# Optimization experiments

Measured on AMD Instinct MI355X. Metric: run time of the kernel, lower is better.

## Reference

```python
import jax, jax.numpy as jnp
import numpy as np
from jax import lax

B, DIM, H, W = 16, 256, 56, 56
HEADS, WIN, K = 8, 4, 5
DH = DIM // HEADS
BN_EPS = 1e-5


def conv2d(x, w, b, stride=1, pad=0, groups=1):
    y = lax.conv_general_dilated(
        x, w, (stride, stride), [(pad, pad), (pad, pad)],
        dimension_numbers=('NCHW', 'OIHW', 'NCHW'), feature_group_count=groups)
    return y + b[None, :, None, None]


def batchnorm(x, g, b, m, v):
    scale = g / jnp.sqrt(v + BN_EPS)
    return (x - m[None, :, None, None]) * scale[None, :, None, None] + b[None, :, None, None]


def setup_inputs() -> dict:
    key = jax.random.key(0)
    ks = jax.random.split(key, 16)
    s = 0.05
    return {
        'x': jax.random.normal(ks[0], (B, DIM, H, W), jnp.float32),
        'q_w': jax.random.normal(ks[1], (DIM, DIM, 1, 1), jnp.float32) * s,
        'q_b': jnp.zeros((DIM,), jnp.float32),
        'kv_w': jax.random.normal(ks[2], (2 * DIM, DIM, 1, 1), jnp.float32) * s,
        'kv_b': jnp.zeros((2 * DIM,), jnp.float32),
        'p0_w': jax.random.normal(ks[3], (DIM, 1, K, K), jnp.float32) * s,
        'p0_b': jnp.zeros((DIM,), jnp.float32),
        'bn0_g': jnp.ones((DIM,), jnp.float32),
        'bn0_b': jnp.zeros((DIM,), jnp.float32),
        'bn0_m': jax.random.normal(ks[4], (DIM,), jnp.float32) * 0.1,
        'bn0_v': jax.random.uniform(ks[5], (DIM,), jnp.float32, 0.5, 1.5),
        'pl0_w': jax.random.normal(ks[6], (DIM, DIM, 1, 1), jnp.float32) * s,
        'pl0_b': jnp.zeros((DIM,), jnp.float32),
        'p1_w': jax.random.normal(ks[7], (DIM, 1, K, K), jnp.float32) * s,
        'p1_b': jnp.zeros((DIM,), jnp.float32),
        'bn1_g': jnp.ones((DIM,), jnp.float32),
        'bn1_b': jnp.zeros((DIM,), jnp.float32),
        'bn1_m': jax.random.normal(ks[8], (DIM,), jnp.float32) * 0.1,
        'bn1_v': jax.random.uniform(ks[9], (DIM,), jnp.float32, 0.5, 1.5),
        'loc_w': jax.random.normal(ks[10], (DIM, 1, K, K), jnp.float32) * s,
        'loc_b': jnp.zeros((DIM,), jnp.float32),
        'mix_w': jax.random.normal(ks[11], (DIM, DIM, 1, 1), jnp.float32) * s,
        'mix_b': jnp.zeros((DIM,), jnp.float32),
    }


def reference(x, q_w, q_b, kv_w, kv_b, p0_w, p0_b, bn0_g, bn0_b, bn0_m, bn0_v,
              pl0_w, pl0_b, p1_w, p1_b, bn1_g, bn1_b, bn1_m, bn1_v,
              loc_w, loc_b, mix_w, mix_b):
    b, c, h, w = x.shape
    scalor = DH ** (-0.5)

    # Q projection (1x1 conv)
    q_local = conv2d(x, q_w, q_b)

    # refined_downsample: (dwconv s2 -> BN -> 1x1) -> (dwconv s2 -> BN)
    p = conv2d(x, p0_w, p0_b, stride=2, pad=K // 2, groups=DIM)
    p = batchnorm(p, bn0_g, bn0_b, bn0_m, bn0_v)
    p = conv2d(p, pl0_w, pl0_b)
    p = conv2d(p, p1_w, p1_b, stride=2, pad=K // 2, groups=DIM)
    p = batchnorm(p, bn1_g, bn1_b, bn1_m, bn1_v)
    Hp, Wp = p.shape[2], p.shape[3]

    # KV projection on pooled map
    kv = conv2d(p, kv_w, kv_b)  # (b, 2*c, Hp, Wp)
    kv = kv.reshape(b, 2, HEADS, DH, Hp * Wp)
    k = kv[:, 0].transpose(0, 1, 3, 2)  # (b, heads, HW, dh)
    v = kv[:, 1].transpose(0, 1, 3, 2)

    q = q_local.reshape(b, HEADS, DH, h * w).transpose(0, 1, 3, 2)  # (b, heads, hw, dh)

    attn = jax.nn.softmax(scalor * jnp.einsum('bnqd,bnkd->bnqk', q, k), axis=-1)
    global_feat = jnp.einsum('bnqk,bnkd->bnqd', attn, v)  # (b, heads, hw, dh)
    global_feat = global_feat.transpose(0, 1, 3, 2).reshape(b, c, h, w)

    # local mixer: depthwise conv (use_lfae=False path)
    local_feat = conv2d(q_local, loc_w, loc_b, pad=K // 2, groups=DIM)
    local_feat = local_feat * jax.nn.sigmoid(local_feat)  # local_weight gating (silu)
    local_feat = local_feat * jax.nn.sigmoid(global_feat)  # local2global gating

    return conv2d(local_feat * global_feat, mix_w, mix_b)
```

## Files before the change

kernel.cpp:

```cpp
#include <hip/hip_runtime.h>
#include <cstdint>

#define BEPS 1e-5f

typedef __attribute__((ext_vector_type(8))) short short8;
typedef __attribute__((ext_vector_type(4))) float f32x4;

static __device__ __forceinline__ uint32_t f2bf(float f) {
    union { float f; uint32_t u; } v; v.f = f;
    return (v.u + 0x7FFFu + ((v.u >> 16) & 1u)) >> 16;
}
static __device__ __forceinline__ uint32_t pk2(float lo, float hi) {
    return (f2bf(hi) << 16) | (f2bf(lo) & 0xFFFFu);
}

__global__ __launch_bounds__(256) void gemm1x1_mfma(
    const float* __restrict__ in, const float* __restrict__ w,
    const float* __restrict__ bias, float* __restrict__ out,
    int Ci, int Co, int P)
{
    const int b  = blockIdx.z;
    const int p0 = blockIdx.x * 128;
    const int c0 = blockIdx.y * 128;
    const int tid  = threadIdx.x;
    const int lane = tid & 63;
    const int wave = tid >> 6;
    const int wm = wave >> 1, wn = wave & 1;
    const int l15 = lane & 15;
    const int kg  = lane >> 4;

    __shared__ short sA[128][40];
    __shared__ short sB[128][40];

    f32x4 acc[4][4] = {};

    const float* inb = in + (size_t)b * Ci * P;

    const int arow  = tid >> 1;
    const int ahalf = (tid & 1) * 16;
    const int bp    = tid & 127;
    const int bhalf = (tid >> 7) * 16;
    const bool bok  = (p0 + bp) < P;

    for (int k0 = 0; k0 < Ci; k0 += 32) {
        {
            const float* src = &w[(size_t)(c0 + arow) * Ci + k0 + ahalf];
            float4 f0 = *(const float4*)(src + 0);
            float4 f1 = *(const float4*)(src + 4);
            float4 f2 = *(const float4*)(src + 8);
            float4 f3 = *(const float4*)(src + 12);
            uint4 q0, q1;
            q0.x = pk2(f0.x, f0.y); q0.y = pk2(f0.z, f0.w);
            q0.z = pk2(f1.x, f1.y); q0.w = pk2(f1.z, f1.w);
            q1.x = pk2(f2.x, f2.y); q1.y = pk2(f2.z, f2.w);
            q1.z = pk2(f3.x, f3.y); q1.w = pk2(f3.z, f3.w);
            *(uint4*)&sA[arow][ahalf]     = q0;
            *(uint4*)&sA[arow][ahalf + 8] = q1;
        }
        {
            const float* src = &inb[(size_t)(k0 + bhalf) * P + p0 + bp];
            float fv[16];
#pragma unroll
            for (int i = 0; i < 16; ++i)
                fv[i] = bok ? src[(size_t)i * P] : 0.f;
            uint4 q0, q1;
            q0.x = pk2(fv[0], fv[1]);  q0.y = pk2(fv[2], fv[3]);
            q0.z = pk2(fv[4], fv[5]);  q0.w = pk2(fv[6], fv[7]);
            q1.x = pk2(fv[8], fv[9]);  q1.y = pk2(fv[10], fv[11]);
            q1.z = pk2(fv[12], fv[13]); q1.w = pk2(fv[14], fv[15]);
            *(uint4*)&sB[bp][bhalf]     = q0;
            *(uint4*)&sB[bp][bhalf + 8] = q1;
        }
        __syncthreads();

        short8 aF[4], bF[4];
#pragma unroll
        for (int m = 0; m < 4; ++m)
            aF[m] = *(const short8*)&sA[wm * 64 + m * 16 + l15][kg * 8];
#pragma unroll
        for (int n = 0; n < 4; ++n)
            bF[n] = *(const short8*)&sB[wn * 64 + n * 16 + l15][kg * 8];
#pragma unroll
        for (int m = 0; m < 4; ++m)
#pragma unroll
            for (int n = 0; n < 4; ++n)
                acc[m][n] = __builtin_amdgcn_mfma_f32_16x16x32_bf16(aF[m], bF[n], acc[m][n], 0, 0, 0);
        __syncthreads();
    }

    float* outb = out + (size_t)b * Co * P;
#pragma unroll
    for (int m = 0; m < 4; ++m) {
        int row = c0 + wm * 64 + m * 16 + kg * 4;
#pragma unroll
        for (int n = 0; n < 4; ++n) {
            int col = p0 + wn * 64 + n * 16 + l15;
            if (col < P) {
#pragma unroll
                for (int j = 0; j < 4; ++j)
                    outb[(size_t)(row + j) * P + col] = acc[m][n][j] + bias[row + j];
            }
        }
    }
}

__global__ __launch_bounds__(256) void dwconv_bn(
    const float* __restrict__ in, const float* __restrict__ w5,
    const float* __restrict__ cb, const float* __restrict__ g,
    const float* __restrict__ bb, const float* __restrict__ m,
    const float* __restrict__ v, float* __restrict__ out,
    int Hin, int Win, int Hout, int Wout, int stride, int total)
{
    int idx = blockIdx.x * 256 + threadIdx.x;
    if (idx >= total) return;
    int x = idx % Wout;
    int t = idx / Wout;
    int y = t % Hout;
    t /= Hout;
    int c = t & 255;
    int b = t >> 8;
    const float* ib = in + (size_t)(b * 256 + c) * Hin * Win;
    const float* wc = w5 + c * 25;
    float s = 0.f;
#pragma unroll
    for (int dy = 0; dy < 5; ++dy) {
        int iy = y * stride + dy - 2;
        if (iy < 0 || iy >= Hin) continue;
#pragma unroll
        for (int dx = 0; dx < 5; ++dx) {
            int ix = x * stride + dx - 2;
            if (ix < 0 || ix >= Win) continue;
            s = fmaf(wc[dy * 5 + dx], ib[iy * Win + ix], s);
        }
    }
    s += cb[c];
    float sc = g[c] * rsqrtf(v[c] + BEPS);
    out[idx] = (s - m[c]) * sc + bb[c];
}

__global__ __launch_bounds__(256, 3) void attn_mfma2(
    const float* __restrict__ qloc,
    const float* __restrict__ kvbuf,
    float* __restrict__ gf)
{
    const int b  = blockIdx.z;
    const int h  = blockIdx.y;
    const int p0 = blockIdx.x * 448;
    const int tid  = threadIdx.x;
    const int lane = tid & 63;
    const int w    = tid >> 6;
    const int l15  = lane & 15;
    const int kg   = lane >> 4;

    __shared__ __align__(16) short sV[32][216];
    __shared__ __align__(16) short sP[4][16][216];

    const float* kp = kvbuf + ((size_t)b * 512 + h * 32) * 196;
    const float* vp = kvbuf + ((size_t)b * 512 + 256 + h * 32) * 196;
    const float* qp = qloc + ((size_t)b * 256 + h * 32) * 3136 + p0;
    float* op = gf + ((size_t)b * 256 + h * 32) * 3136 + p0;

    for (int idx = tid; idx < 32 * 52; idx += 256) {
        int d = idx / 52, c4 = idx - d * 52;
        float4 vv;
        if (c4 < 49) vv = *(const float4*)&vp[d * 196 + c4 * 4];
        else         vv = make_float4(0.f, 0.f, 0.f, 0.f);
        uint2 u2 = make_uint2(pk2(vv.x, vv.y), pk2(vv.z, vv.w));
        *(uint2*)&sV[d][c4 * 4] = u2;
    }

    short8 aK[13];
#pragma unroll
    for (int t = 0; t < 13; ++t) {
        int key = t * 16 + l15;
        float kvv[8];
#pragma unroll
        for (int j = 0; j < 8; ++j)
            kvv[j] = (key < 196) ? kp[(size_t)(kg * 8 + j) * 196 + key] : 0.f;
        union { short8 s; uint32_t u[4]; } pk_;
        pk_.u[0] = pk2(kvv[0], kvv[1]);
        pk_.u[1] = pk2(kvv[2], kvv[3]);
        pk_.u[2] = pk2(kvv[4], kvv[5]);
        pk_.u[3] = pk2(kvv[6], kvv[7]);
        aK[t] = pk_.s;
    }
    __syncthreads();

    const float scal = 0.17677669529663687f;
    const short8 zz = {0, 0, 0, 0, 0, 0, 0, 0};

    float qv[8];
#pragma unroll
    for (int j = 0; j < 8; ++j)
        qv[j] = qp[(size_t)(kg * 8 + j) * 3136 + (w * 7) * 16 + l15];

#pragma unroll
    for (int i = 0; i < 7; ++i) {
        const int qbase = (w * 7 + i) * 16;

        union { short8 s; uint32_t u[4]; } bq;
        bq.u[0] = pk2(qv[0], qv[1]);
        bq.u[1] = pk2(qv[2], qv[3]);
        bq.u[2] = pk2(qv[4], qv[5]);
        bq.u[3] = pk2(qv[6], qv[7]);

        if (i < 6) {
#pragma unroll
            for (int j = 0; j < 8; ++j)
                qv[j] = qp[(size_t)(kg * 8 + j) * 3136 + (w * 7 + i + 1) * 16 + l15];
        }

        f32x4 sAcc[13];
#pragma unroll
        for (int t = 0; t < 13; ++t) {
            f32x4 z = {0.f, 0.f, 0.f, 0.f};
            sAcc[t] = __builtin_amdgcn_mfma_f32_16x16x32_bf16(aK[t], bq.s, z, 0, 0, 0);
        }

        float rsum = 0.f;
#pragma unroll
        for (int t = 0; t < 13; ++t) {
#pragma unroll
            for (int j = 0; j < 4; ++j) {
                int key = t * 16 + kg * 4 + j;
                float e = (key < 196) ? __expf(sAcc[t][j] * scal) : 0.f;
                sAcc[t][j] = e;
                rsum += e;
            }
        }
        rsum += __shfl_xor(rsum, 16);
        rsum += __shfl_xor(rsum, 32);
        float inv = 1.f / rsum;

#pragma unroll
        for (int t = 0; t < 13; ++t) {
            uint64_t v64 = (uint64_t)pk2(sAcc[t][2] * inv, sAcc[t][3] * inv) << 32
                         | (uint64_t)pk2(sAcc[t][0] * inv, sAcc[t][1] * inv);
            *(uint64_t*)&sP[w][l15][t * 16 + kg * 4] = v64;
        }
        asm volatile("s_waitcnt lgkmcnt(0)" ::: "memory");

        f32x4 oAcc[2] = {};
#pragma unroll
        for (int c = 0; c < 7; ++c) {
            int col = c * 32 + kg * 8;
            bool valid = (c < 6) || (kg < 2);
            int cs = valid ? col : 0;
            short8 bP  = *(const short8*)&sP[w][l15][cs];
            short8 aV0 = *(const short8*)&sV[l15][cs];
            short8 aV1 = *(const short8*)&sV[16 + l15][cs];
            if (!valid) bP = zz;
            oAcc[0] = __builtin_amdgcn_mfma_f32_16x16x32_bf16(aV0, bP, oAcc[0], 0, 0, 0);
            oAcc[1] = __builtin_amdgcn_mfma_f32_16x16x32_bf16(aV1, bP, oAcc[1], 0, 0, 0);
        }

        float* ob = op + qbase + l15;
#pragma unroll
        for (int mt = 0; mt < 2; ++mt)
#pragma unroll
            for (int j = 0; j < 4; ++j)
                ob[(size_t)(mt * 16 + kg * 4 + j) * 3136] = oAcc[mt][j];
    }
}

__global__ __launch_bounds__(256) void gate_kernel2(
    const float* __restrict__ ql, const float* __restrict__ w5,
    const float* __restrict__ cb, const float* __restrict__ gfb,
    float* __restrict__ t_out)
{
    const int bc  = blockIdx.x;
    const int c   = bc & 255;
    const int tid = threadIdx.x;

    __shared__ float tile[60][64];

    const float* ib = ql + (size_t)bc * 3136;

    for (int idx = tid; idx < 840; idx += 256) {
        int r = idx / 14, c4 = idx - r * 14;
        int y = r - 2;
        float4 v;
        if (y >= 0 && y < 56) v = *(const float4*)&ib[y * 56 + c4 * 4];
        else                  v = make_float4(0.f, 0.f, 0.f, 0.f);
        float2* dst = (float2*)&tile[r][2 + c4 * 4];
        dst[0] = make_float2(v.x, v.y);
        dst[1] = make_float2(v.z, v.w);
    }
    if (tid < 240) {
        int r = tid >> 2, pc = tid & 3;
        tile[r][(pc < 2) ? pc : 56 + pc] = 0.f;
    }

    float wv[25];
    const float* wc = w5 + c * 25;
#pragma unroll
    for (int i = 0; i < 25; ++i) wv[i] = wc[i];
    const float bias = cb[c];

    __syncthreads();

    const float* gb = gfb + (size_t)bc * 3136;
    float* tb = t_out + (size_t)bc * 3136;

    for (int g = tid; g < 784; g += 256) {
        int y = g / 14, x4 = (g - y * 14) * 4;
        float acc[4] = {bias, bias, bias, bias};
#pragma unroll
        for (int dy = 0; dy < 5; ++dy) {
            float v[8];
            *(float4*)&v[0] = *(const float4*)&tile[y + dy][x4];
            *(float4*)&v[4] = *(const float4*)&tile[y + dy][x4 + 4];
#pragma unroll
            for (int o = 0; o < 4; ++o)
#pragma unroll
                for (int dx = 0; dx < 5; ++dx)
                    acc[o] = fmaf(wv[dy * 5 + dx], v[o + dx], acc[o]);
        }
        float4 gv = *(const float4*)&gb[y * 56 + x4];
        float gvv[4] = {gv.x, gv.y, gv.z, gv.w};
        float ov[4];
#pragma unroll
        for (int o = 0; o < 4; ++o) {
            float s  = acc[o];
            float sl = s / (1.f + __expf(-s));
            float sg = 1.f / (1.f + __expf(-gvv[o]));
            ov[o] = sl * sg * gvv[o];
        }
        *(float4*)&tb[y * 56 + x4] = make_float4(ov[0], ov[1], ov[2], ov[3]);
    }
}

extern "C" void kernel_launch(void* const* d_in, const int* in_sizes, int n_in,
                              void* d_out, int out_size, void* d_ws, size_t ws_size,
                              hipStream_t stream)
{
    const float* x     = (const float*)d_in[0];
    const float* q_w   = (const float*)d_in[1];
    const float* q_b   = (const float*)d_in[2];
    const float* kv_w  = (const float*)d_in[3];
    const float* kv_b  = (const float*)d_in[4];
    const float* p0_w  = (const float*)d_in[5];
    const float* p0_b  = (const float*)d_in[6];
    const float* bn0_g = (const float*)d_in[7];
    const float* bn0_b = (const float*)d_in[8];
    const float* bn0_m = (const float*)d_in[9];
    const float* bn0_v = (const float*)d_in[10];
    const float* pl0_w = (const float*)d_in[11];
    const float* pl0_b = (const float*)d_in[12];
    const float* p1_w  = (const float*)d_in[13];
    const float* p1_b  = (const float*)d_in[14];
    const float* bn1_g = (const float*)d_in[15];
    const float* bn1_b = (const float*)d_in[16];
    const float* bn1_m = (const float*)d_in[17];
    const float* bn1_v = (const float*)d_in[18];
    const float* loc_w = (const float*)d_in[19];
    const float* loc_b = (const float*)d_in[20];
    const float* mix_w = (const float*)d_in[21];
    const float* mix_b = (const float*)d_in[22];

    float* qlocal = (float*)d_out;
    float* ws  = (float*)d_ws;
    float* gf  = ws;
    float* tb  = ws + 12845056;
    float* p0  = tb;
    float* pl0 = tb + 3211264;
    float* p1  = tb + 6422528;
    float* kv  = tb + 7225344;

    gemm1x1_mfma<<<dim3(25, 2, 16), 256, 0, stream>>>(x, q_w, q_b, qlocal, 256, 256, 3136);
    dwconv_bn<<<dim3(12544), 256, 0, stream>>>(x, p0_w, p0_b, bn0_g, bn0_b, bn0_m, bn0_v,
                                               p0, 56, 56, 28, 28, 2, 3211264);
    gemm1x1_mfma<<<dim3(7, 2, 16), 256, 0, stream>>>(p0, pl0_w, pl0_b, pl0, 256, 256, 784);
    dwconv_bn<<<dim3(3136), 256, 0, stream>>>(pl0, p1_w, p1_b, bn1_g, bn1_b, bn1_m, bn1_v,
                                              p1, 28, 28, 14, 14, 2, 802816);
    gemm1x1_mfma<<<dim3(2, 4, 16), 256, 0, stream>>>(p1, kv_w, kv_b, kv, 256, 512, 196);
    attn_mfma2<<<dim3(7, 8, 16), 256, 0, stream>>>(qlocal, kv, gf);
    gate_kernel2<<<dim3(4096), 256, 0, stream>>>(qlocal, loc_w, loc_b, gf, tb);
    gemm1x1_mfma<<<dim3(25, 2, 16), 256, 0, stream>>>(tb, mix_w, mix_b, qlocal, 256, 256, 3136);
}
```

Before: 410.2 us.

## Keep softmax probabilities in registers and permute V layout to match MFMA fragments

The attention kernel no longer stages the probability matrix P through shared memory. Exponentials are packed to bf16 directly from the QK^T MFMA accumulator layout and fed as the B operand of the PV MFMA. V is stored in shared memory with keys permuted to match that register layout. Softmax normalisation is moved to the output, and occupancy is raised to 4 blocks per SM with the outer loop no longer unrolled. The risks are bf16 rounding of unnormalised exponentials and register pressure under the tighter launch bound.

Measured after the change: 478.0 us. 1.17x slower.

```diff
diff --git a/kernel.cpp b/kernel.cpp
--- a/kernel.cpp
+++ b/kernel.cpp
@@ -138,7 +138,7 @@
     out[idx] = (s - m[c]) * sc + bb[c];
 }
 
-__global__ __launch_bounds__(256, 3) void attn_mfma2(
+__global__ __launch_bounds__(256, 4) void attn_mfma3(
     const float* __restrict__ qloc,
     const float* __restrict__ kvbuf,
     float* __restrict__ gf)
@@ -152,21 +152,23 @@
     const int l15  = lane & 15;
     const int kg   = lane >> 4;
 
-    __shared__ __align__(16) short sV[32][216];
-    __shared__ __align__(16) short sP[4][16][216];
+    __shared__ __align__(16) short sVp[32][232];
 
     const float* kp = kvbuf + ((size_t)b * 512 + h * 32) * 196;
     const float* vp = kvbuf + ((size_t)b * 512 + 256 + h * 32) * 196;
     const float* qp = qloc + ((size_t)b * 256 + h * 32) * 3136 + p0;
     float* op = gf + ((size_t)b * 256 + h * 32) * 3136 + p0;
 
-    for (int idx = tid; idx < 32 * 52; idx += 256) {
-        int d = idx / 52, c4 = idx - d * 52;
+    for (int idx = tid; idx < 32 * 58; idx += 256) {
+        int d = idx / 58, g4 = idx - d * 58;
+        int k4 = g4 * 4;
+        int u = k4 >> 5, kl = k4 & 31;
+        int kgs = kl >> 3, jj = kl & 7;
+        int key0 = u * 32 + (jj >= 4 ? 16 : 0) + kgs * 4;
         float4 vv;
-        if (c4 < 49) vv = *(const float4*)&vp[d * 196 + c4 * 4];
-        else         vv = make_float4(0.f, 0.f, 0.f, 0.f);
-        uint2 u2 = make_uint2(pk2(vv.x, vv.y), pk2(vv.z, vv.w));
-        *(uint2*)&sV[d][c4 * 4] = u2;
+        if (key0 < 196) vv = *(const float4*)&vp[d * 196 + key0];
+        else            vv = make_float4(0.f, 0.f, 0.f, 0.f);
+        *(uint2*)&sVp[d][k4] = make_uint2(pk2(vv.x, vv.y), pk2(vv.z, vv.w));
     }
 
     short8 aK[13];
@@ -187,14 +189,12 @@
     __syncthreads();
 
     const float scal = 0.17677669529663687f;
-    const short8 zz = {0, 0, 0, 0, 0, 0, 0, 0};
 
     float qv[8];
 #pragma unroll
     for (int j = 0; j < 8; ++j)
         qv[j] = qp[(size_t)(kg * 8 + j) * 3136 + (w * 7) * 16 + l15];
 
-#pragma unroll
     for (int i = 0; i < 7; ++i) {
         const int qbase = (w * 7 + i) * 16;
 
@@ -210,48 +210,38 @@
                 qv[j] = qp[(size_t)(kg * 8 + j) * 3136 + (w * 7 + i + 1) * 16 + l15];
         }
 
-        f32x4 sAcc[13];
+        uint32_t pq[26];
+        float rsum = 0.f;
 #pragma unroll
         for (int t = 0; t < 13; ++t) {
             f32x4 z = {0.f, 0.f, 0.f, 0.f};
-            sAcc[t] = __builtin_amdgcn_mfma_f32_16x16x32_bf16(aK[t], bq.s, z, 0, 0, 0);
-        }
-
-        float rsum = 0.f;
-#pragma unroll
-        for (int t = 0; t < 13; ++t) {
+            f32x4 s = __builtin_amdgcn_mfma_f32_16x16x32_bf16(aK[t], bq.s, z, 0, 0, 0);
+            float e[4];
 #pragma unroll
             for (int j = 0; j < 4; ++j) {
                 int key = t * 16 + kg * 4 + j;
-                float e = (key < 196) ? __expf(sAcc[t][j] * scal) : 0.f;
-                sAcc[t][j] = e;
-                rsum += e;
+                e[j] = (key < 196) ? __expf(s[j] * scal) : 0.f;
+                rsum += e[j];
             }
+            pq[2 * t]     = pk2(e[0], e[1]);
+            pq[2 * t + 1] = pk2(e[2], e[3]);
         }
         rsum += __shfl_xor(rsum, 16);
         rsum += __shfl_xor(rsum, 32);
         float inv = 1.f / rsum;
 
-#pragma unroll
-        for (int t = 0; t < 13; ++t) {
-            uint64_t v64 = (uint64_t)pk2(sAcc[t][2] * inv, sAcc[t][3] * inv) << 32
-                         | (uint64_t)pk2(sAcc[t][0] * inv, sAcc[t][1] * inv);
-            *(uint64_t*)&sP[w][l15][t * 16 + kg * 4] = v64;
-        }
-        asm volatile("s_waitcnt lgkmcnt(0)" ::: "memory");
-
         f32x4 oAcc[2] = {};
 #pragma unroll
-        for (int c = 0; c < 7; ++c) {
-            int col = c * 32 + kg * 8;
-            bool valid = (c < 6) || (kg < 2);
-            int cs = valid ? col : 0;
-            short8 bP  = *(const short8*)&sP[w][l15][cs];
-            short8 aV0 = *(const short8*)&sV[l15][cs];
-            short8 aV1 = *(const short8*)&sV[16 + l15][cs];
-            if (!valid) bP = zz;
-            oAcc[0] = __builtin_amdgcn_mfma_f32_16x16x32_bf16(aV0, bP, oAcc[0], 0, 0, 0);
-            oAcc[1] = __builtin_amdgcn_mfma_f32_16x16x32_bf16(aV1, bP, oAcc[1], 0, 0, 0);
+        for (int u = 0; u < 7; ++u) {
+            union { short8 s; uint32_t w[4]; } bP;
+            bP.w[0] = pq[4 * u];
+            bP.w[1] = pq[4 * u + 1];
+            bP.w[2] = (u < 6) ? pq[4 * u + 2] : 0u;
+            bP.w[3] = (u < 6) ? pq[4 * u + 3] : 0u;
+            short8 aV0 = *(const short8*)&sVp[l15][u * 32 + kg * 8];
+            short8 aV1 = *(const short8*)&sVp[16 + l15][u * 32 + kg * 8];
+            oAcc[0] = __builtin_amdgcn_mfma_f32_16x16x32_bf16(aV0, bP.s, oAcc[0], 0, 0, 0);
+            oAcc[1] = __builtin_amdgcn_mfma_f32_16x16x32_bf16(aV1, bP.s, oAcc[1], 0, 0, 0);
         }
 
         float* ob = op + qbase + l15;
@@ -259,7 +249,7 @@
         for (int mt = 0; mt < 2; ++mt)
 #pragma unroll
             for (int j = 0; j < 4; ++j)
-                ob[(size_t)(mt * 16 + kg * 4 + j) * 3136] = oAcc[mt][j];
+                ob[(size_t)(mt * 16 + kg * 4 + j) * 3136] = oAcc[mt][j] * inv;
     }
 }
 
@@ -374,7 +364,7 @@
     dwconv_bn<<<dim3(3136), 256, 0, stream>>>(pl0, p1_w, p1_b, bn1_g, bn1_b, bn1_m, bn1_v,
                                               p1, 28, 28, 14, 14, 2, 802816);
     gemm1x1_mfma<<<dim3(2, 4, 16), 256, 0, stream>>>(p1, kv_w, kv_b, kv, 256, 512, 196);
-    attn_mfma2<<<dim3(7, 8, 16), 256, 0, stream>>>(qlocal, kv, gf);
+    attn_mfma3<<<dim3(7, 8, 16), 256, 0, stream>>>(qlocal, kv, gf);
     gate_kernel2<<<dim3(4096), 256, 0, stream>>>(qlocal, loc_w, loc_b, gf, tb);
     gemm1x1_mfma<<<dim3(25, 2, 16), 256, 0, stream>>>(tb, mix_w, mix_b, qlocal, 256, 256, 3136);
 }
```
